# Kernel tuning notes

Measured on AMD Instinct MI355X. Metric: run time of the kernel, lower is better.

Reference implementation:

```python
import jax, jax.numpy as jnp
import numpy as np

N_NODES = 20000
N_EDGES = 320000
F_IN = 128
H = 4        # heads per layer
D = 128      # per-head hidden dim
NEG_SLOPE = 0.2


def setup_inputs() -> dict:
    key = jax.random.key(0)
    ks = jax.random.split(key, 14)
    s = 0.05
    inp = {
        "feats": jax.random.normal(ks[0], (N_NODES, F_IN), jnp.float32),
        "src": jax.random.randint(ks[1], (N_EDGES,), 0, N_NODES, jnp.int64),
        "dst": jax.random.randint(ks[2], (N_EDGES,), 0, N_NODES, jnp.int64),
        # layer 1: in F_IN -> H heads x D, flatten agg
        "W1": s * jax.random.normal(ks[3], (F_IN, H * D), jnp.float32),
        "al1": s * jax.random.normal(ks[4], (H, D), jnp.float32),
        "ar1": s * jax.random.normal(ks[5], (H, D), jnp.float32),
        "b1": jnp.zeros((H * D,), jnp.float32),
        # layer 2: in H*D -> H heads x D, mean agg
        "W2": s * jax.random.normal(ks[6], (H * D, H * D), jnp.float32),
        "al2": s * jax.random.normal(ks[7], (H, D), jnp.float32),
        "ar2": s * jax.random.normal(ks[8], (H, D), jnp.float32),
        "b2": jnp.zeros((H * D,), jnp.float32),
        # readout Linear(D, 1)
        "Wr": s * jax.random.normal(ks[9], (D, 1), jnp.float32),
        "br": jnp.zeros((1,), jnp.float32),
    }
    return inp


def _gat_conv(x, src, dst, W, al, ar, b, n_nodes):
    """dgl GATConv: per-head linear, edge softmax over incoming edges, scatter-sum."""
    h, d = al.shape
    z = (x @ W).reshape(n_nodes, h, d)                      # [N,H,D]
    el = jnp.einsum('nhd,hd->nh', z, al)                    # [N,H]
    er = jnp.einsum('nhd,hd->nh', z, ar)                    # [N,H]
    e = jax.nn.leaky_relu(el[src] + er[dst], NEG_SLOPE)     # [E,H]
    # numerically stable softmax grouped by destination node
    emax = jax.lax.stop_gradient(jax.ops.segment_max(e, dst, num_segments=n_nodes))
    a = jnp.exp(e - emax[dst])                              # [E,H]
    denom = jax.ops.segment_sum(a, dst, num_segments=n_nodes)
    alpha = a / jnp.maximum(denom[dst], 1e-9)               # [E,H]
    out = jax.ops.segment_sum(alpha[:, :, None] * z[src], dst, num_segments=n_nodes)
    return out + b.reshape(1, h, d)                         # [N,H,D]


def reference(feats, src, dst, W1, al1, ar1, b1, W2, al2, ar2, b2, Wr, br):
    n = feats.shape[0]
    h1 = _gat_conv(feats, src, dst, W1, al1, ar1, b1, n)    # [N,H,D]
    h1 = jax.nn.elu(h1.reshape(n, -1))                      # flatten heads -> [N,H*D]
    h2 = _gat_conv(h1, src, dst, W2, al2, ar2, b2, n)       # [N,H,D]
    h2 = h2.mean(axis=1)                                    # mean over heads -> [N,D]
    node_preds = h2 @ Wr + br                               # [N,1]
    return node_preds.sum(axis=0)                           # [1]
```

## Files before the change

kernel.cpp:

```cpp
#include <hip/hip_runtime.h>
#include <hip/hip_bf16.h>
#include <cstddef>

constexpr int NN = 20000;
constexpr int NE = 320000;
constexpr int NHEAD = 4;
constexpr int HD = 512;
constexpr int MPAD = 20096;
constexpr int SLOTS = 64;
constexpr float NEG_SLOPE = 0.2f;

using short8 = __attribute__((ext_vector_type(8))) short;
using f32x4 = __attribute__((ext_vector_type(4))) float;

__device__ inline void gload16(const void* g, void* l) {
  __builtin_amdgcn_global_load_lds(
      (const __attribute__((address_space(1))) void*)g,
      (__attribute__((address_space(3))) void*)l, 16, 0, 0);
}

__device__ inline float fastrcp(float x) { return __builtin_amdgcn_rcpf(x); }

__device__ inline float fast_elu(float x) {
  return (x > 0.f) ? x : (__expf(x) - 1.0f);
}

constexpr int S0 = NN;
constexpr int S1 = S0 + NN * 128 / 4;
constexpr int S2 = S1 + 512 * 128;
constexpr int S3 = S2 + 4 * 16 * 128;
constexpr int S4 = S3 + 1024;
constexpr int S5 = S4 + 60000;
constexpr int S6 = S5 + 256;
__global__ __launch_bounds__(256) void prep_kernel(
    const float* __restrict__ feats, const float* __restrict__ W1,
    const float* __restrict__ W2, const float* __restrict__ al1,
    const float* __restrict__ ar1, const float* __restrict__ al2,
    const float* __restrict__ ar2, const float* __restrict__ Wr,
    __hip_bfloat16* __restrict__ featsb, __hip_bfloat16* __restrict__ W1t,
    __hip_bfloat16* __restrict__ vcombh, float* __restrict__ wl1t,
    float* __restrict__ wr1t, float* __restrict__ zero3,
    float* __restrict__ partials, int* __restrict__ cnt) {
  int t = blockIdx.x * 256 + threadIdx.x;
  if (t < S0) {
    cnt[t] = 0;
  } else if (t < S1) {
    int u = (t - S0) * 4;
    float4 f = *reinterpret_cast<const float4*>(&feats[u]);
    __hip_bfloat162 o0 = __float22bfloat162_rn(make_float2(f.x, f.y));
    __hip_bfloat162 o1 = __float22bfloat162_rn(make_float2(f.z, f.w));
    uint2 pk;
    pk.x = *reinterpret_cast<unsigned int*>(&o0);
    pk.y = *reinterpret_cast<unsigned int*>(&o1);
    *reinterpret_cast<uint2*>(&featsb[u]) = pk;
  } else if (t < S2) {
    int u = t - S1;
    W1t[u] = __float2bfloat16(W1[(size_t)(u & 127) * 512 + (u >> 7)]);
  } else if (t < S3) {
    int u = t - S2;
    int head = u >> 11, rem = u & 2047;
    int m = rem >> 7, kk = rem & 127;
    float s = 0.f;
    if (m < 12) {
      int h = m & 3;
      const float* vec = (m < 4) ? (al2 + h * 128)
                       : (m < 8) ? (ar2 + h * 128) : Wr;
      const float* wrow = W2 + (size_t)(head * 128 + kk) * 512 + h * 128;
      for (int d = 0; d < 128; ++d) s += wrow[d] * vec[d];
    }
    int slot = kk >> 3, e = kk & 7;
    int sl = slot ^ (m & 7);
    vcombh[head * 2048 + m * 128 + sl * 8 + e] = __float2bfloat16(s);
  } else if (t < S4) {
    int u = t - S3;
    int d = u >> 3, rem = u & 7, h = rem >> 1, sel = rem & 1;
    const float* vec = (sel ? ar1 : al1) + h * 128;
    const float* wrow = W1 + (size_t)d * 512 + h * 128;
    float s = 0.f;
    for (int dd = 0; dd < 128; ++dd) s += wrow[dd] * vec[dd];
    (sel ? wr1t : wl1t)[d * 4 + h] = s;
  } else if (t < S5) {
    int u = (t - S4) * 4;
    *reinterpret_cast<float4*>(&zero3[u]) = make_float4(0.f, 0.f, 0.f, 0.f);
  } else if (t < S6) {
    partials[t - S5] = 0.f;
  }
}

__global__ __launch_bounds__(256) void fill_logits_kernel(
    const int* __restrict__ src, const int* __restrict__ dst,
    int* __restrict__ cnt, int* __restrict__ src_perm,
    const __hip_bfloat16* __restrict__ featsb,
    const float* __restrict__ wl1t, const float* __restrict__ wr1t,
    float* __restrict__ el1, float* __restrict__ er1) {
  int t = threadIdx.x;
  {
    int nth = gridDim.x * 256;
    int gid = blockIdx.x * 256 + t;
    for (int e = gid; e < NE; e += nth) {
      int d = dst[e];
      int p = atomicAdd(&cnt[d], 1);
      if (p < SLOTS) src_perm[d * SLOTS + p] = src[e];
    }
  }
  int wv = t >> 6, lane = t & 63;
  int n = blockIdx.x * 4 + wv;
  unsigned int uu = *reinterpret_cast<const unsigned int*>(
      &featsb[(size_t)n * 128 + 2 * lane]);
  __hip_bfloat162 ub = *reinterpret_cast<__hip_bfloat162*>(&uu);
  float2 f = __bfloat1622float2(ub);
  float4 wlA = *reinterpret_cast<const float4*>(&wl1t[lane * 8]);
  float4 wlB = *reinterpret_cast<const float4*>(&wl1t[lane * 8 + 4]);
  float4 wrA = *reinterpret_cast<const float4*>(&wr1t[lane * 8]);
  float4 wrB = *reinterpret_cast<const float4*>(&wr1t[lane * 8 + 4]);
  float p0 = f.x * wlA.x + f.y * wlB.x;
  float p1 = f.x * wlA.y + f.y * wlB.y;
  float p2 = f.x * wlA.z + f.y * wlB.z;
  float p3 = f.x * wlA.w + f.y * wlB.w;
  float p4 = f.x * wrA.x + f.y * wrB.x;
  float p5 = f.x * wrA.y + f.y * wrB.y;
  float p6 = f.x * wrA.z + f.y * wrB.z;
  float p7 = f.x * wrA.w + f.y * wrB.w;
#pragma unroll
  for (int off = 1; off < 64; off <<= 1) {
    p0 += __shfl_xor(p0, off); p1 += __shfl_xor(p1, off);
    p2 += __shfl_xor(p2, off); p3 += __shfl_xor(p3, off);
    p4 += __shfl_xor(p4, off); p5 += __shfl_xor(p5, off);
    p6 += __shfl_xor(p6, off); p7 += __shfl_xor(p7, off);
  }
  if (lane == 0) {
    *reinterpret_cast<float4*>(&el1[n * 4]) = make_float4(p0, p1, p2, p3);
    *reinterpret_cast<float4*>(&er1[n * 4]) = make_float4(p4, p5, p6, p7);
  }
}

__global__ __launch_bounds__(256) void gather_kernel(
    const __hip_bfloat16* __restrict__ featsb,
    const int* __restrict__ cnt, const int* __restrict__ src_perm,
    const float* __restrict__ el, const float* __restrict__ er,
    __hip_bfloat16* __restrict__ aggb) {
  __shared__ float4 alph[4][SLOTS];
  __shared__ int srcb[4][SLOTS];
  int wv = __builtin_amdgcn_readfirstlane((int)(threadIdx.x >> 6));
  int n = blockIdx.x * 4 + wv;
  int lane = threadIdx.x & 63;
  int c = min(cnt[n], SLOTS);

  {
    float4 er4 = *reinterpret_cast<const float4*>(&er[n * 4]);
    float a0 = 0.f, a1 = 0.f, a2 = 0.f, a3 = 0.f;
    int sv = 0;
    if (lane < c) {
      sv = src_perm[n * SLOTS + lane];
      float4 e4 = *reinterpret_cast<const float4*>(&el[sv * 4]);
      float x0 = e4.x + er4.x, x1 = e4.y + er4.y;
      float x2 = e4.z + er4.z, x3 = e4.w + er4.w;
      x0 = (x0 > 0.f) ? x0 : NEG_SLOPE * x0;
      x1 = (x1 > 0.f) ? x1 : NEG_SLOPE * x1;
      x2 = (x2 > 0.f) ? x2 : NEG_SLOPE * x2;
      x3 = (x3 > 0.f) ? x3 : NEG_SLOPE * x3;
      a0 = __expf(x0); a1 = __expf(x1); a2 = __expf(x2); a3 = __expf(x3);
    }
    float s0 = a0, s1 = a1, s2 = a2, s3 = a3;
#pragma unroll
    for (int off = 1; off < 64; off <<= 1) {
      s0 += __shfl_xor(s0, off);
      s1 += __shfl_xor(s1, off);
      s2 += __shfl_xor(s2, off);
      s3 += __shfl_xor(s3, off);
    }
    float i0 = fastrcp(fmaxf(s0, 1e-9f));
    float i1 = fastrcp(fmaxf(s1, 1e-9f));
    float i2 = fastrcp(fmaxf(s2, 1e-9f));
    float i3 = fastrcp(fmaxf(s3, 1e-9f));
    alph[wv][lane] = make_float4(a0 * i0, a1 * i1, a2 * i2, a3 * i3);
    srcb[wv][lane] = sv;
  }

  float acc[4][2] = {};

#define EB(IDX)                                                                \
  {                                                                            \
    float4 a4 = alph[wv][(IDX)];                                               \
    int s = srcb[wv][(IDX)];                                                   \
    unsigned int uu = *reinterpret_cast<const unsigned int*>(                  \
        &featsb[(size_t)s * 128 + 2 * lane]);                                  \
    __hip_bfloat162 ub = *reinterpret_cast<__hip_bfloat162*>(&uu);             \
    float2 f = __bfloat1622float2(ub);                                         \
    acc[0][0] += a4.x * f.x; acc[0][1] += a4.x * f.y;                          \
    acc[1][0] += a4.y * f.x; acc[1][1] += a4.y * f.y;                          \
    acc[2][0] += a4.z * f.x; acc[2][1] += a4.z * f.y;                          \
    acc[3][0] += a4.w * f.x; acc[3][1] += a4.w * f.y;                          \
  }

  int i = 0;
  for (; i + 3 < c; i += 4) {
    EB(i) EB(i + 1) EB(i + 2) EB(i + 3)
  }
  for (; i < c; ++i) EB(i)
#undef EB

  size_t obase = (size_t)n * HD + 2 * lane;
#pragma unroll
  for (int h = 0; h < 4; ++h) {
    __hip_bfloat162 o = __float22bfloat162_rn(make_float2(acc[h][0], acc[h][1]));
    *reinterpret_cast<unsigned int*>(&aggb[obase + h * 128]) =
        *reinterpret_cast<unsigned int*>(&o);
  }
}

__global__ __launch_bounds__(256) void h1_gemm_kernel(
    const __hip_bfloat16* __restrict__ A,
    const __hip_bfloat16* __restrict__ Bt,
    const __hip_bfloat16* __restrict__ vcombh,
    const float* __restrict__ b1,
    float* __restrict__ el2, float* __restrict__ er2,
    float* __restrict__ q2) {
  __shared__ short AsH[64 * 128];
  __shared__ short Bs[128 * 128];
  __shared__ short Vc[16 * 128];
  int t = threadIdx.x;
  int lane = t & 63, wave = t >> 6;
  int rowBase = blockIdx.x * 64;
  int head = blockIdx.y;
  int nloc = lane & 15;
  int quad = lane >> 4;

#pragma unroll
  for (int p = 0; p < 4; ++p) {
    int fbase = p * 256 + wave * 64;
    int f = fbase + lane;
    int row = f >> 4, slot = f & 15;
    int ss = slot ^ (row & 7);
    gload16(A + (size_t)(rowBase + row) * HD + head * 128 + ss * 8,
            AsH + fbase * 8);
  }
#pragma unroll
  for (int p = 0; p < 8; ++p) {
    int fbase = p * 256 + wave * 64;
    int f = fbase + lane;
    int row = f >> 4, slot = f & 15;
    int ss = slot ^ (row & 7);
    gload16(Bt + (size_t)(head * 128 + row) * 128 + ss * 8,
            Bs + fbase * 8);
  }
  {
    int fbase = wave * 64;
    gload16(vcombh + head * 2048 + (size_t)(fbase + lane) * 8,
            Vc + fbase * 8);
  }
  __syncthreads();

  f32x4 acc[8];
#pragma unroll
  for (int i = 0; i < 8; ++i) acc[i] = (f32x4){0.f, 0.f, 0.f, 0.f};
#pragma unroll
  for (int c = 0; c < 4; ++c) {
    int arow = wave * 16 + nloc;
    short8 bfr = *(const short8*)&AsH[arow * 128 +
                                      (((c << 2) + quad) ^ (arow & 7)) * 8];
#pragma unroll
    for (int i = 0; i < 8; ++i) {
      int brow = i * 16 + nloc;
      short8 af = *(const short8*)&Bs[brow * 128 +
                                      (((c << 2) + quad) ^ (brow & 7)) * 8];
      acc[i] = __builtin_amdgcn_mfma_f32_16x16x32_bf16(af, bfr, acc[i], 0, 0, 0);
    }
  }

  int node = wave * 16 + nloc;
#pragma unroll
  for (int i = 0; i < 8; ++i) {
    float4 b4 = *reinterpret_cast<const float4*>(
        &b1[head * 128 + i * 16 + quad * 4]);
    float e0 = fast_elu(acc[i][0] + b4.x);
    float e1 = fast_elu(acc[i][1] + b4.y);
    float e2 = fast_elu(acc[i][2] + b4.z);
    float e3 = fast_elu(acc[i][3] + b4.w);
    __hip_bfloat162 p0 = __float22bfloat162_rn(make_float2(e0, e1));
    __hip_bfloat162 p1 = __float22bfloat162_rn(make_float2(e2, e3));
    uint2 pk;
    pk.x = *reinterpret_cast<unsigned int*>(&p0);
    pk.y = *reinterpret_cast<unsigned int*>(&p1);
    int slot = i * 2 + (quad >> 1);
    int sub = quad & 1;
    int sl = slot ^ (node & 7);
    *reinterpret_cast<uint2*>(&AsH[node * 128 + sl * 8 + sub * 4]) = pk;
  }

  f32x4 acc2 = (f32x4){0.f, 0.f, 0.f, 0.f};
#pragma unroll
  for (int c = 0; c < 4; ++c) {
    short8 a2 = *(const short8*)&Vc[nloc * 128 +
                                    (((c << 2) + quad) ^ (nloc & 7)) * 8];
    short8 b2 = *(const short8*)&AsH[node * 128 +
                                     (((c << 2) + quad) ^ (node & 7)) * 8];
    acc2 = __builtin_amdgcn_mfma_f32_16x16x32_bf16(a2, b2, acc2, 0, 0, 0);
  }

  int gn = rowBase + node;
  if (gn < NN && quad < 3) {
    float* dp = (quad == 0) ? el2 : (quad == 1) ? er2 : q2;
#pragma unroll
    for (int r = 0; r < 4; ++r)
      atomicAdd(&dp[(size_t)gn * 4 + r], acc2[r]);
  }
}

__global__ __launch_bounds__(256) void attn_q_kernel(
    const int* __restrict__ src_perm,
    const int* __restrict__ cnt,
    const float* __restrict__ el,
    const float* __restrict__ er,
    const float* __restrict__ q,
    float* __restrict__ partials) {
  __shared__ float blk[4];
  int wv = __builtin_amdgcn_readfirstlane((int)(threadIdx.x >> 6));
  int n = blockIdx.x * 4 + wv;
  int lane = threadIdx.x & 63;
  int c = min(cnt[n], SLOTS);
  float4 er4 = *reinterpret_cast<const float4*>(&er[n * 4]);
  float a0 = 0.f, a1 = 0.f, a2 = 0.f, a3 = 0.f;
  int s = 0;
  if (lane < c) {
    s = src_perm[n * SLOTS + lane];
    float4 e4 = *reinterpret_cast<const float4*>(&el[s * 4]);
    float x0 = e4.x + er4.x, x1 = e4.y + er4.y;
    float x2 = e4.z + er4.z, x3 = e4.w + er4.w;
    x0 = (x0 > 0.f) ? x0 : NEG_SLOPE * x0;
    x1 = (x1 > 0.f) ? x1 : NEG_SLOPE * x1;
    x2 = (x2 > 0.f) ? x2 : NEG_SLOPE * x2;
    x3 = (x3 > 0.f) ? x3 : NEG_SLOPE * x3;
    a0 = __expf(x0); a1 = __expf(x1); a2 = __expf(x2); a3 = __expf(x3);
  }
  float s0 = a0, s1 = a1, s2 = a2, s3 = a3;
#pragma unroll
  for (int off = 1; off < 64; off <<= 1) {
    s0 += __shfl_xor(s0, off);
    s1 += __shfl_xor(s1, off);
    s2 += __shfl_xor(s2, off);
    s3 += __shfl_xor(s3, off);
  }
  float p = 0.f;
  if (lane < c) {
    float4 q4 = *reinterpret_cast<const float4*>(&q[s * 4]);
    p = (a0 * fastrcp(fmaxf(s0, 1e-9f))) * q4.x +
        (a1 * fastrcp(fmaxf(s1, 1e-9f))) * q4.y +
        (a2 * fastrcp(fmaxf(s2, 1e-9f))) * q4.z +
        (a3 * fastrcp(fmaxf(s3, 1e-9f))) * q4.w;
  }
#pragma unroll
  for (int off = 32; off > 0; off >>= 1) p += __shfl_down(p, off);
  if (lane == 0) blk[wv] = p;
  __syncthreads();
  if (threadIdx.x == 0) {
    atomicAdd(&partials[blockIdx.x & 255], blk[0] + blk[1] + blk[2] + blk[3]);
  }
}

__global__ __launch_bounds__(512) void final_kernel(
    const float* __restrict__ partials, const float* __restrict__ b2,
    const float* __restrict__ Wr, const float* __restrict__ br,
    float* __restrict__ out) {
  __shared__ float tmp[512];
  int t = threadIdx.x;
  float sum = (t < 256) ? partials[t] : 0.f;
  sum += (float)NN * b2[t] * Wr[t & 127];
  tmp[t] = sum;
  __syncthreads();
  for (int off = 256; off > 0; off >>= 1) {
    if (t < off) tmp[t] += tmp[t + off];
    __syncthreads();
  }
  if (t == 0) out[0] = 0.25f * tmp[0] + (float)NN * br[0];
}

extern "C" void kernel_launch(void* const* d_in, const int* in_sizes, int n_in,
                              void* d_out, int out_size, void* d_ws, size_t ws_size,
                              hipStream_t stream) {
  const float* feats = (const float*)d_in[0];
  const int* src = (const int*)d_in[1];
  const int* dst = (const int*)d_in[2];
  const float* W1 = (const float*)d_in[3];
  const float* al1 = (const float*)d_in[4];
  const float* ar1 = (const float*)d_in[5];
  const float* b1 = (const float*)d_in[6];
  const float* W2 = (const float*)d_in[7];
  const float* al2 = (const float*)d_in[8];
  const float* ar2 = (const float*)d_in[9];
  const float* b2 = (const float*)d_in[10];
  const float* Wr = (const float*)d_in[11];
  const float* br = (const float*)d_in[12];
  float* out = (float*)d_out;

  __hip_bfloat16* featsb = (__hip_bfloat16*)d_ws;
  __hip_bfloat16* aggb = featsb + (size_t)NN * 128;
  __hip_bfloat16* W1t = aggb + (size_t)MPAD * HD;
  __hip_bfloat16* vcombh = W1t + 512 * 128;
  float* wl1t = (float*)(vcombh + 4 * 16 * 128);
  float* wr1t = wl1t + 512;
  float* el1 = wr1t + 512;
  float* er1 = el1 + (size_t)NN * NHEAD;
  float* el2 = er1 + (size_t)NN * NHEAD;
  float* er2 = el2 + (size_t)NN * NHEAD;
  float* q2 = er2 + (size_t)NN * NHEAD;
  float* partials = q2 + (size_t)NN * NHEAD;
  int* cnt = (int*)(partials + 256);
  int* src_perm = cnt + NN;

  prep_kernel<<<(S6 + 255) / 256, 256, 0, stream>>>(
      feats, W1, W2, al1, ar1, al2, ar2, Wr, featsb, W1t, vcombh, wl1t, wr1t,
      el2, partials, cnt);

  fill_logits_kernel<<<NN / 4, 256, 0, stream>>>(
      src, dst, cnt, src_perm, featsb, wl1t, wr1t, el1, er1);

  gather_kernel<<<NN / 4, 256, 0, stream>>>(featsb, cnt, src_perm, el1, er1,
                                            aggb);

  dim3 h1grid(MPAD / 64, NHEAD);
  h1_gemm_kernel<<<h1grid, 256, 0, stream>>>(aggb, W1t, vcombh, b1, el2,
                                             er2, q2);

  attn_q_kernel<<<NN / 4, 256, 0, stream>>>(src_perm, cnt, el2, er2, q2,
                                            partials);
  final_kernel<<<1, 512, 0, stream>>>(partials, b2, Wr, br, out);
}
```

Baseline: 164.7 us.

## Replace per-head atomics with per-head partial buffers and drop final reduction kernel

The GEMM kernel now writes per-head logit and q contributions to a [head][node][16] partial buffer with plain vector stores instead of float atomics into zero-initialised el2/er2/q2. The attention kernel sums the four head partials on read and atomically accumulates straight into the output. Since the head sums are resolved on read, the zeroing in prep and the separate final reduction kernel are no longer needed. The bias term is folded into prep by one thread writing the initial output value. This removes one launch, the zeroing work and the atomic traffic, at the cost of four times more gathered reads per edge and heavy atomic contention on a single output address.

New measurement: 218.4 us. 1.33x slower.

```diff
diff --git a/kernel.cpp b/kernel.cpp
--- a/kernel.cpp
+++ b/kernel.cpp
@@ -30,17 +30,17 @@
 constexpr int S2 = S1 + 512 * 128;
 constexpr int S3 = S2 + 4 * 16 * 128;
 constexpr int S4 = S3 + 1024;
-constexpr int S5 = S4 + 60000;
-constexpr int S6 = S5 + 256;
+constexpr int S5 = S4 + 1;
 __global__ __launch_bounds__(256) void prep_kernel(
     const float* __restrict__ feats, const float* __restrict__ W1,
     const float* __restrict__ W2, const float* __restrict__ al1,
     const float* __restrict__ ar1, const float* __restrict__ al2,
     const float* __restrict__ ar2, const float* __restrict__ Wr,
+    const float* __restrict__ b2, const float* __restrict__ br,
     __hip_bfloat16* __restrict__ featsb, __hip_bfloat16* __restrict__ W1t,
     __hip_bfloat16* __restrict__ vcombh, float* __restrict__ wl1t,
-    float* __restrict__ wr1t, float* __restrict__ zero3,
-    float* __restrict__ partials, int* __restrict__ cnt) {
+    float* __restrict__ wr1t, int* __restrict__ cnt,
+    float* __restrict__ out) {
   int t = blockIdx.x * 256 + threadIdx.x;
   if (t < S0) {
     cnt[t] = 0;
@@ -80,10 +80,9 @@
     for (int dd = 0; dd < 128; ++dd) s += wrow[dd] * vec[dd];
     (sel ? wr1t : wl1t)[d * 4 + h] = s;
   } else if (t < S5) {
-    int u = (t - S4) * 4;
-    *reinterpret_cast<float4*>(&zero3[u]) = make_float4(0.f, 0.f, 0.f, 0.f);
-  } else if (t < S6) {
-    partials[t - S5] = 0.f;
+    float dot = 0.f;
+    for (int i = 0; i < 512; ++i) dot += b2[i] * Wr[i & 127];
+    out[0] = 0.25f * (float)NN * dot + (float)NN * br[0];
   }
 }
 
@@ -214,8 +213,7 @@
     const __hip_bfloat16* __restrict__ Bt,
     const __hip_bfloat16* __restrict__ vcombh,
     const float* __restrict__ b1,
-    float* __restrict__ el2, float* __restrict__ er2,
-    float* __restrict__ q2) {
+    float* __restrict__ part) {
   __shared__ short AsH[64 * 128];
   __shared__ short Bs[128 * 128];
   __shared__ short Vc[16 * 128];
@@ -299,32 +297,41 @@
   }
 
   int gn = rowBase + node;
-  if (gn < NN && quad < 3) {
-    float* dp = (quad == 0) ? el2 : (quad == 1) ? er2 : q2;
-#pragma unroll
-    for (int r = 0; r < 4; ++r)
-      atomicAdd(&dp[(size_t)gn * 4 + r], acc2[r]);
-  }
+  float4 st = make_float4(acc2[0], acc2[1], acc2[2], acc2[3]);
+  *reinterpret_cast<float4*>(
+      &part[(((size_t)head * MPAD + gn) << 4) + (quad << 2)]) = st;
 }
 
 __global__ __launch_bounds__(256) void attn_q_kernel(
     const int* __restrict__ src_perm,
     const int* __restrict__ cnt,
-    const float* __restrict__ el,
-    const float* __restrict__ er,
-    const float* __restrict__ q,
-    float* __restrict__ partials) {
+    const float* __restrict__ part,
+    float* __restrict__ out) {
   __shared__ float blk[4];
   int wv = __builtin_amdgcn_readfirstlane((int)(threadIdx.x >> 6));
   int n = blockIdx.x * 4 + wv;
   int lane = threadIdx.x & 63;
   int c = min(cnt[n], SLOTS);
-  float4 er4 = *reinterpret_cast<const float4*>(&er[n * 4]);
+  float4 er4 = make_float4(0.f, 0.f, 0.f, 0.f);
+#pragma unroll
+  for (int h = 0; h < 4; ++h) {
+    float4 tr = *reinterpret_cast<const float4*>(
+        &part[(((size_t)h * MPAD + n) << 4) + 4]);
+    er4.x += tr.x; er4.y += tr.y; er4.z += tr.z; er4.w += tr.w;
+  }
   float a0 = 0.f, a1 = 0.f, a2 = 0.f, a3 = 0.f;
-  int s = 0;
+  float4 q4 = make_float4(0.f, 0.f, 0.f, 0.f);
   if (lane < c) {
-    s = src_perm[n * SLOTS + lane];
-    float4 e4 = *reinterpret_cast<const float4*>(&el[s * 4]);
+    int s = src_perm[n * SLOTS + lane];
+    float4 e4 = make_float4(0.f, 0.f, 0.f, 0.f);
+#pragma unroll
+    for (int h = 0; h < 4; ++h) {
+      const float* pb = &part[((size_t)h * MPAD + s) << 4];
+      float4 te = *reinterpret_cast<const float4*>(pb);
+      float4 tq = *reinterpret_cast<const float4*>(pb + 8);
+      e4.x += te.x; e4.y += te.y; e4.z += te.z; e4.w += te.w;
+      q4.x += tq.x; q4.y += tq.y; q4.z += tq.z; q4.w += tq.w;
+    }
     float x0 = e4.x + er4.x, x1 = e4.y + er4.y;
     float x2 = e4.z + er4.z, x3 = e4.w + er4.w;
     x0 = (x0 > 0.f) ? x0 : NEG_SLOPE * x0;
@@ -343,7 +350,6 @@
   }
   float p = 0.f;
   if (lane < c) {
-    float4 q4 = *reinterpret_cast<const float4*>(&q[s * 4]);
     p = (a0 * fastrcp(fmaxf(s0, 1e-9f))) * q4.x +
         (a1 * fastrcp(fmaxf(s1, 1e-9f))) * q4.y +
         (a2 * fastrcp(fmaxf(s2, 1e-9f))) * q4.z +
@@ -354,25 +360,8 @@
   if (lane == 0) blk[wv] = p;
   __syncthreads();
   if (threadIdx.x == 0) {
-    atomicAdd(&partials[blockIdx.x & 255], blk[0] + blk[1] + blk[2] + blk[3]);
-  }
-}
-
-__global__ __launch_bounds__(512) void final_kernel(
-    const float* __restrict__ partials, const float* __restrict__ b2,
-    const float* __restrict__ Wr, const float* __restrict__ br,
-    float* __restrict__ out) {
-  __shared__ float tmp[512];
-  int t = threadIdx.x;
-  float sum = (t < 256) ? partials[t] : 0.f;
-  sum += (float)NN * b2[t] * Wr[t & 127];
-  tmp[t] = sum;
-  __syncthreads();
-  for (int off = 256; off > 0; off >>= 1) {
-    if (t < off) tmp[t] += tmp[t + off];
-    __syncthreads();
-  }
-  if (t == 0) out[0] = 0.25f * tmp[0] + (float)NN * br[0];
+    atomicAdd(out, 0.25f * (blk[0] + blk[1] + blk[2] + blk[3]));
+  }
 }
 
 extern "C" void kernel_launch(void* const* d_in, const int* in_sizes, int n_in,
@@ -401,16 +390,13 @@
   float* wr1t = wl1t + 512;
   float* el1 = wr1t + 512;
   float* er1 = el1 + (size_t)NN * NHEAD;
-  float* el2 = er1 + (size_t)NN * NHEAD;
-  float* er2 = el2 + (size_t)NN * NHEAD;
-  float* q2 = er2 + (size_t)NN * NHEAD;
-  float* partials = q2 + (size_t)NN * NHEAD;
-  int* cnt = (int*)(partials + 256);
+  float* part = er1 + (size_t)NN * NHEAD;
+  int* cnt = (int*)(part + (size_t)4 * MPAD * 16);
   int* src_perm = cnt + NN;
 
-  prep_kernel<<<(S6 + 255) / 256, 256, 0, stream>>>(
-      feats, W1, W2, al1, ar1, al2, ar2, Wr, featsb, W1t, vcombh, wl1t, wr1t,
-      el2, partials, cnt);
+  prep_kernel<<<(S5 + 255) / 256, 256, 0, stream>>>(
+      feats, W1, W2, al1, ar1, al2, ar2, Wr, b2, br, featsb, W1t, vcombh,
+      wl1t, wr1t, cnt, out);
 
   fill_logits_kernel<<<NN / 4, 256, 0, stream>>>(
       src, dst, cnt, src_perm, featsb, wl1t, wr1t, el1, er1);
@@ -419,10 +405,7 @@
                                             aggb);
 
   dim3 h1grid(MPAD / 64, NHEAD);
-  h1_gemm_kernel<<<h1grid, 256, 0, stream>>>(aggb, W1t, vcombh, b1, el2,
-                                             er2, q2);
-
-  attn_q_kernel<<<NN / 4, 256, 0, stream>>>(src_perm, cnt, el2, er2, q2,
-                                            partials);
-  final_kernel<<<1, 512, 0, stream>>>(partials, b2, Wr, br, out);
-}
+  h1_gemm_kernel<<<h1grid, 256, 0, stream>>>(aggb, W1t, vcombh, b1, part);
+
+  attn_q_kernel<<<NN / 4, 256, 0, stream>>>(src_perm, cnt, part, out);
+}
```
